# Kernel optimization log

Measured on AMD Instinct MI355X. Metric: run time of the kernel, lower is better.

Reference implementation:

```python
import jax, jax.numpy as jnp
import numpy as np

SQ, SK, D = 8192, 8192, 128

def setup_inputs() -> dict:
    k = jax.random.key(0)
    kq, kk, kv = jax.random.split(k, 3)
    query = jax.random.normal(kq, (SQ, D), dtype=jnp.float32)
    key = jax.random.normal(kk, (SK, D), dtype=jnp.float32)
    value = jax.random.normal(kv, (SK, D), dtype=jnp.float32)
    return {"query": query, "key": key, "value": value}

def reference(query, key, value):
    # attn_weights = dot_general(q, k, contract last dims) -> [Sq, Sk]
    attn_weights = jnp.einsum('qd,kd->qk', query, key)
    # softmax over key dims (second half of attn_weights dims)
    attn_weights = jax.nn.softmax(attn_weights, axis=-1)
    # dropout is identity: train=False -> deterministic
    # y = dot_general(attn_weights, value, contract key dims) -> [Sq, Dv]
    y = jnp.einsum('qk,kd->qd', attn_weights, value)
    return y
```

## Files before the change

kernel.cpp:

```cpp
#include <hip/hip_runtime.h>
#include <hip/hip_bf16.h>
#include <stdint.h>

#define SQ 8192
#define SK 8192
#define DH 128
#define NIT 32
#define L2E 1.4426950408889634f
#define CB 40.0f

typedef __attribute__((ext_vector_type(8))) _Float16 f16x8;
typedef __attribute__((ext_vector_type(8))) short bf16x8;
typedef __attribute__((ext_vector_type(16))) float f32x16;
typedef __attribute__((ext_vector_type(4))) short s16x4;
typedef __attribute__((ext_vector_type(4))) unsigned int u32x4;

__device__ __forceinline__ short f2h(float f) {
  _Float16 h = (_Float16)f;
  return __builtin_bit_cast(short, h);
}
__device__ __forceinline__ short f2bf(float f) {
  uint32_t u = __builtin_bit_cast(uint32_t, f);
  u = (u + 0x7FFFu + ((u >> 16) & 1u)) >> 16;
  return (short)u;
}

__global__ __launch_bounds__(256) void prep_kernel(const float* __restrict__ K,
                                                   const float* __restrict__ V,
                                                   short* __restrict__ Kimg,
                                                   short* __restrict__ Vimg) {
  __shared__ short T[32][136];
  const int tid = threadIdx.x;
  if (blockIdx.x < 256) {
    const int kb = blockIdx.x;
#pragma unroll
    for (int i = 0; i < 2; ++i) {
      int ci = i * 256 + tid;
      int kc = ci >> 6, lane = ci & 63;
      int key = kb * 32 + (lane & 31);
      int k0 = kc * 16 + (lane >> 5) * 8;
      const float* src = K + (size_t)key * DH + k0;
      float4 a = *(const float4*)src;
      float4 b = *(const float4*)(src + 4);
      s16x4 o0, o1;
      o0.x = f2h(a.x); o0.y = f2h(a.y); o0.z = f2h(a.z); o0.w = f2h(a.w);
      o1.x = f2h(b.x); o1.y = f2h(b.y); o1.z = f2h(b.z); o1.w = f2h(b.w);
      s16x4* dst = (s16x4*)(Kimg + (size_t)kb * 4096 + ci * 8);
      dst[0] = o0; dst[1] = o1;
    }
  } else {
    const int kb = blockIdx.x - 256;
#pragma unroll
    for (int i = 0; i < 4; ++i) {
      int fi = i * 256 + tid;
      int key = fi >> 5;
      int dc = (fi & 31) * 4;
      float4 v = ((const float4*)V)[(size_t)(kb * 32 + key) * (DH / 4) + (fi & 31)];
      T[key][dc + 0] = f2bf(v.x); T[key][dc + 1] = f2bf(v.y);
      T[key][dc + 2] = f2bf(v.z); T[key][dc + 3] = f2bf(v.w);
    }
    __syncthreads();
#pragma unroll
    for (int i = 0; i < 2; ++i) {
      int ci = i * 256 + tid;
      int lane = ci & 63;
      int g = ci >> 6;
      int dt = g & 3, ks = g >> 2;
      int base = ks * 16 + (lane >> 5) * 4;
      int d = dt * 32 + (lane & 31);
      s16x4 o0, o1;
      o0.x = T[base + 0][d]; o0.y = T[base + 1][d];
      o0.z = T[base + 2][d]; o0.w = T[base + 3][d];
      o1.x = T[base + 8][d]; o1.y = T[base + 9][d];
      o1.z = T[base + 10][d]; o1.w = T[base + 11][d];
      s16x4* dst = (s16x4*)(Vimg + (size_t)kb * 4096 + ci * 8);
      dst[0] = o0; dst[1] = o1;
    }
  }
}

__global__ __launch_bounds__(512, 2) void attn_kernel(const float* __restrict__ Q,
                                                      const short* __restrict__ Kimg,
                                                      const short* __restrict__ Vimg,
                                                      float* __restrict__ out) {
  __shared__ __align__(16) char smem[67584];
  const int tid = threadIdx.x;
  const int w = tid >> 6;
  const int lane = tid & 63;
  const int half = lane >> 5;
  const int l32 = lane & 31;
  const int qrow0 = blockIdx.x * 32;

  f16x8 qf[8];
  {
    const float* qp = Q + (size_t)(qrow0 + l32) * DH + half * 8;
#pragma unroll
    for (int kc = 0; kc < 8; ++kc) {
      float4 a = *(const float4*)(qp + kc * 16);
      float4 b = *(const float4*)(qp + kc * 16 + 4);
      f16x8 h;
      h[0] = (_Float16)a.x; h[1] = (_Float16)a.y; h[2] = (_Float16)a.z; h[3] = (_Float16)a.w;
      h[4] = (_Float16)b.x; h[5] = (_Float16)b.y; h[6] = (_Float16)b.z; h[7] = (_Float16)b.w;
      qf[kc] = h;
    }
  }

  f32x16 of[4];
#pragma unroll
  for (int dt = 0; dt < 4; ++dt)
#pragma unroll
    for (int c = 0; c < 16; ++c) of[dt][c] = 0.f;
  float l_lane = 0.f;

  f16x8 kf[8];
  bf16x8 vf[8];

  {
    const short* kp = Kimg + (size_t)w * 4096;
    const short* vp = Vimg + (size_t)w * 4096;
#pragma unroll
    for (int kc = 0; kc < 8; ++kc) kf[kc] = *(const f16x8*)(kp + kc * 512 + lane * 8);
#pragma unroll
    for (int g = 0; g < 8; ++g) vf[g] = *(const bf16x8*)(vp + g * 512 + lane * 8);
  }

  for (int t = 0; t < NIT; ++t) {
    f32x16 sacc;
#pragma unroll
    for (int c = 0; c < 16; ++c) sacc[c] = 0.f;
#pragma unroll
    for (int kc = 0; kc < 8; ++kc)
      sacc = __builtin_amdgcn_mfma_f32_32x32x16_f16(kf[kc], qf[kc], sacc, 0, 0, 0);

    if (t + 1 < NIT) {
      const short* kp = Kimg + (size_t)((t + 1) * 8 + w) * 4096;
#pragma unroll
      for (int kc = 0; kc < 8; ++kc) kf[kc] = *(const f16x8*)(kp + kc * 512 + lane * 8);
    }

    u32x4 pav0, pav1;
#pragma unroll
    for (int r = 0; r < 4; ++r) {
      float pA = __builtin_amdgcn_exp2f(fmaf(sacc[2 * r], L2E, -CB));
      float pB = __builtin_amdgcn_exp2f(fmaf(sacc[2 * r + 1], L2E, -CB));
      float pC = __builtin_amdgcn_exp2f(fmaf(sacc[8 + 2 * r], L2E, -CB));
      float pD = __builtin_amdgcn_exp2f(fmaf(sacc[8 + 2 * r + 1], L2E, -CB));
      l_lane += (pA + pB) + (pC + pD);
      uint32_t uA = __builtin_bit_cast(uint32_t, pA); uA += 0x7FFFu + ((uA >> 16) & 1u);
      uint32_t uB = __builtin_bit_cast(uint32_t, pB); uB += 0x7FFFu + ((uB >> 16) & 1u);
      uint32_t uC = __builtin_bit_cast(uint32_t, pC); uC += 0x7FFFu + ((uC >> 16) & 1u);
      uint32_t uD = __builtin_bit_cast(uint32_t, pD); uD += 0x7FFFu + ((uD >> 16) & 1u);
      pav0[r] = __builtin_amdgcn_perm(uB, uA, 0x07060302u);
      pav1[r] = __builtin_amdgcn_perm(uD, uC, 0x07060302u);
    }
    bf16x8 pa0 = __builtin_bit_cast(bf16x8, pav0);
    bf16x8 pa1 = __builtin_bit_cast(bf16x8, pav1);

#pragma unroll
    for (int dt = 0; dt < 4; ++dt) {
      of[dt] = __builtin_amdgcn_mfma_f32_32x32x16_bf16(pa0, vf[dt], of[dt], 0, 0, 0);
      of[dt] = __builtin_amdgcn_mfma_f32_32x32x16_bf16(pa1, vf[4 + dt], of[dt], 0, 0, 0);
    }

    if (t + 1 < NIT) {
      const short* vp = Vimg + (size_t)((t + 1) * 8 + w) * 4096;
#pragma unroll
      for (int g = 0; g < 8; ++g) vf[g] = *(const bf16x8*)(vp + g * 512 + lane * 8);
    }
  }

  float l_tot = l_lane + __shfl_xor(l_lane, 32);

  __syncthreads();
  float* mO = (float*)smem;
  float* R = mO + (w & 3) * 4224;
  if (w < 4) {
#pragma unroll
    for (int c = 0; c < 16; ++c) {
      const int row = (c & 3) + 8 * (c >> 2) + 4 * half;
      float* br = R + row * 132;
#pragma unroll
      for (int dt = 0; dt < 4; ++dt) br[dt * 32 + l32] = of[dt][c];
    }
    if (half == 0) R[l32 * 132 + 128] = l_tot;
  }
  __syncthreads();
  if (w >= 4) {
#pragma unroll
    for (int c = 0; c < 16; ++c) {
      const int row = (c & 3) + 8 * (c >> 2) + 4 * half;
      float* br = R + row * 132;
#pragma unroll
      for (int dt = 0; dt < 4; ++dt) br[dt * 32 + l32] += of[dt][c];
    }
    if (half == 0) R[l32 * 132 + 128] += l_tot;
  }
  __syncthreads();
  {
    const int row = tid >> 4;
    const int cg = tid & 15;
    float den = mO[row * 132 + 128] + mO[4224 + row * 132 + 128] +
                mO[8448 + row * 132 + 128] + mO[12672 + row * 132 + 128];
    float inv = 1.f / den;
    float4 s0 = {0.f, 0.f, 0.f, 0.f}, s1 = {0.f, 0.f, 0.f, 0.f};
#pragma unroll
    for (int rg = 0; rg < 4; ++rg) {
      const float* p = mO + rg * 4224 + row * 132 + cg * 8;
      float4 a = *(const float4*)p;
      float4 b = *(const float4*)(p + 4);
      s0.x += a.x; s0.y += a.y; s0.z += a.z; s0.w += a.w;
      s1.x += b.x; s1.y += b.y; s1.z += b.z; s1.w += b.w;
    }
    s0.x *= inv; s0.y *= inv; s0.z *= inv; s0.w *= inv;
    s1.x *= inv; s1.y *= inv; s1.z *= inv; s1.w *= inv;
    float* op = out + (size_t)(qrow0 + row) * DH + cg * 8;
    *(float4*)op = s0;
    *(float4*)(op + 4) = s1;
  }
}

extern "C" void kernel_launch(void* const* d_in, const int* in_sizes, int n_in,
                              void* d_out, int out_size, void* d_ws, size_t ws_size,
                              hipStream_t stream) {
  const float* Q = (const float*)d_in[0];
  const float* K = (const float*)d_in[1];
  const float* V = (const float*)d_in[2];
  float* out = (float*)d_out;
  short* Kimg = (short*)d_ws;
  short* Vimg = (short*)d_ws + (size_t)SK * DH;
  prep_kernel<<<512, 256, 0, stream>>>(K, V, Kimg, Vimg);
  attn_kernel<<<SQ / 32, 512, 0, stream>>>(Q, Kimg, Vimg, out);
}
```

Before: 110.8 us.

## Split keys across blocks, share K tiles via LDS, add combine kernel

Each block now handles 64 query rows over half the key range. Two query groups of waves share K tiles that are staged into LDS with double-buffered global_load_lds, which halves K global traffic per query row. Partial outputs and row sums are written to the workspace, and a separate combine kernel merges them and normalises. The change also splits the QK MFMA chain into two independent accumulators and raises wave priority around the MFMA sections. In exchange it adds a per-iteration __syncthreads, V loads that are no longer prefetched, an extra kernel launch, and extra global traffic for the partial results.

```diff
diff --git a/kernel.cpp b/kernel.cpp
--- a/kernel.cpp
+++ b/kernel.cpp
@@ -23,6 +23,12 @@
   uint32_t u = __builtin_bit_cast(uint32_t, f);
   u = (u + 0x7FFFu + ((u >> 16) & 1u)) >> 16;
   return (short)u;
+}
+
+__device__ __forceinline__ void gl_lds16(const void* g, void* l) {
+  __builtin_amdgcn_global_load_lds(
+      (const __attribute__((address_space(1))) void*)g,
+      (__attribute__((address_space(3))) void*)l, 16, 0, 0);
 }
 
 __global__ __launch_bounds__(256) void prep_kernel(const float* __restrict__ K,
@@ -79,17 +85,26 @@
   }
 }
 
-__global__ __launch_bounds__(512, 2) void attn_kernel(const float* __restrict__ Q,
-                                                      const short* __restrict__ Kimg,
-                                                      const short* __restrict__ Vimg,
-                                                      float* __restrict__ out) {
+__global__ __launch_bounds__(512, 2) void attn_split(const float* __restrict__ Q,
+                                                     const short* __restrict__ Kimg,
+                                                     const short* __restrict__ Vimg,
+                                                     float* __restrict__ Oa,
+                                                     float* __restrict__ Ob,
+                                                     float* __restrict__ l0,
+                                                     float* __restrict__ l1) {
   __shared__ __align__(16) char smem[67584];
+  short* stg = (short*)smem;
   const int tid = threadIdx.x;
   const int w = tid >> 6;
   const int lane = tid & 63;
   const int half = lane >> 5;
   const int l32 = lane & 31;
-  const int qrow0 = blockIdx.x * 32;
+  const int qh = w >> 2;
+  const int ks = w & 3;
+  const int qb = blockIdx.x >> 1;
+  const int kh = blockIdx.x & 1;
+  const int qrow0 = qb * 64 + qh * 32;
+  const int kb0 = kh * 128;
 
   f16x8 qf[8];
   {
@@ -112,31 +127,49 @@
     for (int c = 0; c < 16; ++c) of[dt][c] = 0.f;
   float l_lane = 0.f;
 
-  f16x8 kf[8];
-  bf16x8 vf[8];
-
-  {
-    const short* kp = Kimg + (size_t)w * 4096;
-    const short* vp = Vimg + (size_t)w * 4096;
-#pragma unroll
-    for (int kc = 0; kc < 8; ++kc) kf[kc] = *(const f16x8*)(kp + kc * 512 + lane * 8);
-#pragma unroll
-    for (int g = 0; g < 8; ++g) vf[g] = *(const bf16x8*)(vp + g * 512 + lane * 8);
-  }
+  const short* gK = Kimg + ((size_t)kb0 + (w >> 1)) * 4096 + (w & 1) * 2048 + lane * 8;
+  short* lK = stg + (w >> 1) * 4096 + (w & 1) * 2048;
+
+  auto STAGE = [&](int c, int t) {
+    const short* g = gK + (size_t)t * 16384;
+    short* l = lK + c * 16384;
+#pragma unroll
+    for (int j = 0; j < 4; ++j)
+      gl_lds16(g + j * 512, l + j * 512);
+  };
+
+  STAGE(0, 0);
+  __syncthreads();
+  int cur = 0;
 
   for (int t = 0; t < NIT; ++t) {
+    bf16x8 vf[8];
+    {
+      const short* vp = Vimg + ((size_t)kb0 + t * 4 + ks) * 4096 + lane * 8;
+#pragma unroll
+      for (int g2 = 0; g2 < 8; ++g2) vf[g2] = *(const bf16x8*)(vp + g2 * 512);
+    }
+
+    const short* bk = stg + cur * 16384 + ks * 4096 + lane * 8;
+    f16x8 kf[8];
+#pragma unroll
+    for (int kc = 0; kc < 8; ++kc) kf[kc] = *(const f16x8*)(bk + kc * 512);
+
+    if (t + 1 < NIT) STAGE(cur ^ 1, t + 1);
+
+    f32x16 sa, sb;
+#pragma unroll
+    for (int c = 0; c < 16; ++c) { sa[c] = 0.f; sb[c] = 0.f; }
+    __builtin_amdgcn_s_setprio(1);
+#pragma unroll
+    for (int kc = 0; kc < 4; ++kc) {
+      sa = __builtin_amdgcn_mfma_f32_32x32x16_f16(kf[kc], qf[kc], sa, 0, 0, 0);
+      sb = __builtin_amdgcn_mfma_f32_32x32x16_f16(kf[4 + kc], qf[4 + kc], sb, 0, 0, 0);
+    }
+    __builtin_amdgcn_s_setprio(0);
     f32x16 sacc;
 #pragma unroll
-    for (int c = 0; c < 16; ++c) sacc[c] = 0.f;
-#pragma unroll
-    for (int kc = 0; kc < 8; ++kc)
-      sacc = __builtin_amdgcn_mfma_f32_32x32x16_f16(kf[kc], qf[kc], sacc, 0, 0, 0);
-
-    if (t + 1 < NIT) {
-      const short* kp = Kimg + (size_t)((t + 1) * 8 + w) * 4096;
-#pragma unroll
-      for (int kc = 0; kc < 8; ++kc) kf[kc] = *(const f16x8*)(kp + kc * 512 + lane * 8);
-    }
+    for (int c = 0; c < 16; ++c) sacc[c] = sa[c] + sb[c];
 
     u32x4 pav0, pav1;
 #pragma unroll
@@ -156,25 +189,24 @@
     bf16x8 pa0 = __builtin_bit_cast(bf16x8, pav0);
     bf16x8 pa1 = __builtin_bit_cast(bf16x8, pav1);
 
+    __builtin_amdgcn_s_setprio(1);
 #pragma unroll
     for (int dt = 0; dt < 4; ++dt) {
       of[dt] = __builtin_amdgcn_mfma_f32_32x32x16_bf16(pa0, vf[dt], of[dt], 0, 0, 0);
       of[dt] = __builtin_amdgcn_mfma_f32_32x32x16_bf16(pa1, vf[4 + dt], of[dt], 0, 0, 0);
     }
-
-    if (t + 1 < NIT) {
-      const short* vp = Vimg + (size_t)((t + 1) * 8 + w) * 4096;
-#pragma unroll
-      for (int g = 0; g < 8; ++g) vf[g] = *(const bf16x8*)(vp + g * 512 + lane * 8);
-    }
+    __builtin_amdgcn_s_setprio(0);
+
+    __syncthreads();
+    cur ^= 1;
   }
 
   float l_tot = l_lane + __shfl_xor(l_lane, 32);
 
   __syncthreads();
   float* mO = (float*)smem;
-  float* R = mO + (w & 3) * 4224;
-  if (w < 4) {
+  float* R = mO + (qh * 2 + (ks & 1)) * 4224;
+  if (ks < 2) {
 #pragma unroll
     for (int c = 0; c < 16; ++c) {
       const int row = (c & 3) + 8 * (c >> 2) + 4 * half;
@@ -185,7 +217,7 @@
     if (half == 0) R[l32 * 132 + 128] = l_tot;
   }
   __syncthreads();
-  if (w >= 4) {
+  if (ks >= 2) {
 #pragma unroll
     for (int c = 0; c < 16; ++c) {
       const int row = (c & 3) + 8 * (c >> 2) + 4 * half;
@@ -197,26 +229,40 @@
   }
   __syncthreads();
   {
-    const int row = tid >> 4;
-    const int cg = tid & 15;
-    float den = mO[row * 132 + 128] + mO[4224 + row * 132 + 128] +
-                mO[8448 + row * 132 + 128] + mO[12672 + row * 132 + 128];
-    float inv = 1.f / den;
-    float4 s0 = {0.f, 0.f, 0.f, 0.f}, s1 = {0.f, 0.f, 0.f, 0.f};
-#pragma unroll
-    for (int rg = 0; rg < 4; ++rg) {
-      const float* p = mO + rg * 4224 + row * 132 + cg * 8;
-      float4 a = *(const float4*)p;
-      float4 b = *(const float4*)(p + 4);
-      s0.x += a.x; s0.y += a.y; s0.z += a.z; s0.w += a.w;
-      s1.x += b.x; s1.y += b.y; s1.z += b.z; s1.w += b.w;
-    }
-    s0.x *= inv; s0.y *= inv; s0.z *= inv; s0.w *= inv;
-    s1.x *= inv; s1.y *= inv; s1.z *= inv; s1.w *= inv;
-    float* op = out + (size_t)(qrow0 + row) * DH + cg * 8;
-    *(float4*)op = s0;
-    *(float4*)(op + 4) = s1;
-  }
+    const int row = tid >> 3;
+    const int cg = tid & 7;
+    const int qh2 = row >> 5;
+    const int r32 = row & 31;
+    const float* Ra = mO + (qh2 * 2 + 0) * 4224 + r32 * 132;
+    const float* Rb = mO + (qh2 * 2 + 1) * 4224 + r32 * 132;
+    float lp = Ra[128] + Rb[128];
+    float* dst = (kh ? Ob : Oa) + (size_t)(qb * 64 + row) * DH + cg * 16;
+#pragma unroll
+    for (int k = 0; k < 4; ++k) {
+      float4 a = *(const float4*)(Ra + cg * 16 + k * 4);
+      float4 b = *(const float4*)(Rb + cg * 16 + k * 4);
+      a.x += b.x; a.y += b.y; a.z += b.z; a.w += b.w;
+      *(float4*)(dst + k * 4) = a;
+    }
+    if (cg == 0) (kh ? l1 : l0)[qb * 64 + row] = lp;
+  }
+}
+
+__global__ __launch_bounds__(256) void combine_kernel(float* __restrict__ Oa,
+                                                      const float* __restrict__ Ob,
+                                                      const float* __restrict__ l0,
+                                                      const float* __restrict__ l1) {
+  const int idx = blockIdx.x * 256 + threadIdx.x;
+  const int row = idx >> 5;
+  const int c4 = (idx & 31) * 4;
+  const float inv = 1.f / (l0[row] + l1[row]);
+  float* pa = Oa + (size_t)row * DH + c4;
+  const float* pb = Ob + (size_t)row * DH + c4;
+  float4 a = *(const float4*)pa;
+  float4 b = *(const float4*)pb;
+  a.x = (a.x + b.x) * inv; a.y = (a.y + b.y) * inv;
+  a.z = (a.z + b.z) * inv; a.w = (a.w + b.w) * inv;
+  *(float4*)pa = a;
 }
 
 extern "C" void kernel_launch(void* const* d_in, const int* in_sizes, int n_in,
@@ -226,8 +272,13 @@
   const float* K = (const float*)d_in[1];
   const float* V = (const float*)d_in[2];
   float* out = (float*)d_out;
-  short* Kimg = (short*)d_ws;
-  short* Vimg = (short*)d_ws + (size_t)SK * DH;
+  char* ws = (char*)d_ws;
+  short* Kimg = (short*)ws;
+  short* Vimg = (short*)(ws + 2097152);
+  float* Ob = (float*)(ws + 4194304);
+  float* l0 = (float*)(ws + 8388608);
+  float* l1 = l0 + SQ;
   prep_kernel<<<512, 256, 0, stream>>>(K, V, Kimg, Vimg);
-  attn_kernel<<<SQ / 32, 512, 0, stream>>>(Q, Kimg, Vimg, out);
-}
+  attn_split<<<SQ / 64 * 2, 512, 0, stream>>>(Q, Kimg, Vimg, out, Ob, l0, l1);
+  combine_kernel<<<SQ * DH / 4 / 256, 256, 0, stream>>>(out, Ob, l0, l1);
+}
```

Result: slower. 118.9 us (+7.4%).

## Split key range across two blocks per query tile and combine partials

Applied to the files above, without the earlier changes.

The attention kernel now splits the key sequence into two halves. Each half is handled by its own workgroup, which doubles the grid to 512 blocks so the 256 compute units are better occupied. Each block writes unnormalized partial outputs and row sums, and a new combine kernel adds the two halves and normalizes. This works without rescaling because the softmax uses a fixed offset rather than a running max. The cost is an extra launch, plus global traffic for the partial outputs and sums, and launch bounds are raised to 4 waves-per-EU hint.

```diff
diff --git a/kernel.cpp b/kernel.cpp
--- a/kernel.cpp
+++ b/kernel.cpp
@@ -5,7 +5,7 @@
 #define SQ 8192
 #define SK 8192
 #define DH 128
-#define NIT 32
+#define NIT 16
 #define L2E 1.4426950408889634f
 #define CB 40.0f
 
@@ -79,17 +79,24 @@
   }
 }
 
-__global__ __launch_bounds__(512, 2) void attn_kernel(const float* __restrict__ Q,
-                                                      const short* __restrict__ Kimg,
-                                                      const short* __restrict__ Vimg,
-                                                      float* __restrict__ out) {
+__global__ __launch_bounds__(512, 4) void attn_split(const float* __restrict__ Q,
+                                                     const short* __restrict__ Kimg,
+                                                     const short* __restrict__ Vimg,
+                                                     float* __restrict__ Oa,
+                                                     float* __restrict__ Ob,
+                                                     float* __restrict__ l0,
+                                                     float* __restrict__ l1) {
   __shared__ __align__(16) char smem[67584];
   const int tid = threadIdx.x;
   const int w = tid >> 6;
   const int lane = tid & 63;
   const int half = lane >> 5;
   const int l32 = lane & 31;
-  const int qrow0 = blockIdx.x * 32;
+  const int b = blockIdx.x;
+  const int kh = (b >> 2) & 1;
+  const int qb = (b >> 3) * 4 + (b & 3);
+  const int qrow0 = qb * 32;
+  const int kb0 = kh * 128;
 
   f16x8 qf[8];
   {
@@ -97,10 +104,10 @@
 #pragma unroll
     for (int kc = 0; kc < 8; ++kc) {
       float4 a = *(const float4*)(qp + kc * 16);
-      float4 b = *(const float4*)(qp + kc * 16 + 4);
+      float4 b2 = *(const float4*)(qp + kc * 16 + 4);
       f16x8 h;
       h[0] = (_Float16)a.x; h[1] = (_Float16)a.y; h[2] = (_Float16)a.z; h[3] = (_Float16)a.w;
-      h[4] = (_Float16)b.x; h[5] = (_Float16)b.y; h[6] = (_Float16)b.z; h[7] = (_Float16)b.w;
+      h[4] = (_Float16)b2.x; h[5] = (_Float16)b2.y; h[6] = (_Float16)b2.z; h[7] = (_Float16)b2.w;
       qf[kc] = h;
     }
   }
@@ -116,8 +123,8 @@
   bf16x8 vf[8];
 
   {
-    const short* kp = Kimg + (size_t)w * 4096;
-    const short* vp = Vimg + (size_t)w * 4096;
+    const short* kp = Kimg + (size_t)(kb0 + w) * 4096;
+    const short* vp = Vimg + (size_t)(kb0 + w) * 4096;
 #pragma unroll
     for (int kc = 0; kc < 8; ++kc) kf[kc] = *(const f16x8*)(kp + kc * 512 + lane * 8);
 #pragma unroll
@@ -133,7 +140,7 @@
       sacc = __builtin_amdgcn_mfma_f32_32x32x16_f16(kf[kc], qf[kc], sacc, 0, 0, 0);
 
     if (t + 1 < NIT) {
-      const short* kp = Kimg + (size_t)((t + 1) * 8 + w) * 4096;
+      const short* kp = Kimg + (size_t)(kb0 + (t + 1) * 8 + w) * 4096;
 #pragma unroll
       for (int kc = 0; kc < 8; ++kc) kf[kc] = *(const f16x8*)(kp + kc * 512 + lane * 8);
     }
@@ -163,7 +170,7 @@
     }
 
     if (t + 1 < NIT) {
-      const short* vp = Vimg + (size_t)((t + 1) * 8 + w) * 4096;
+      const short* vp = Vimg + (size_t)(kb0 + (t + 1) * 8 + w) * 4096;
 #pragma unroll
       for (int g = 0; g < 8; ++g) vf[g] = *(const bf16x8*)(vp + g * 512 + lane * 8);
     }
@@ -199,24 +206,39 @@
   {
     const int row = tid >> 4;
     const int cg = tid & 15;
-    float den = mO[row * 132 + 128] + mO[4224 + row * 132 + 128] +
-                mO[8448 + row * 132 + 128] + mO[12672 + row * 132 + 128];
-    float inv = 1.f / den;
+    float lp = mO[row * 132 + 128] + mO[4224 + row * 132 + 128] +
+               mO[8448 + row * 132 + 128] + mO[12672 + row * 132 + 128];
     float4 s0 = {0.f, 0.f, 0.f, 0.f}, s1 = {0.f, 0.f, 0.f, 0.f};
 #pragma unroll
     for (int rg = 0; rg < 4; ++rg) {
       const float* p = mO + rg * 4224 + row * 132 + cg * 8;
       float4 a = *(const float4*)p;
-      float4 b = *(const float4*)(p + 4);
+      float4 b2 = *(const float4*)(p + 4);
       s0.x += a.x; s0.y += a.y; s0.z += a.z; s0.w += a.w;
-      s1.x += b.x; s1.y += b.y; s1.z += b.z; s1.w += b.w;
-    }
-    s0.x *= inv; s0.y *= inv; s0.z *= inv; s0.w *= inv;
-    s1.x *= inv; s1.y *= inv; s1.z *= inv; s1.w *= inv;
-    float* op = out + (size_t)(qrow0 + row) * DH + cg * 8;
+      s1.x += b2.x; s1.y += b2.y; s1.z += b2.z; s1.w += b2.w;
+    }
+    float* op = (kh ? Ob : Oa) + (size_t)(qrow0 + row) * DH + cg * 8;
     *(float4*)op = s0;
     *(float4*)(op + 4) = s1;
-  }
+    if (cg == 0) (kh ? l1 : l0)[qrow0 + row] = lp;
+  }
+}
+
+__global__ __launch_bounds__(256) void combine_kernel(float* __restrict__ Oa,
+                                                      const float* __restrict__ Ob,
+                                                      const float* __restrict__ l0,
+                                                      const float* __restrict__ l1) {
+  const int idx = blockIdx.x * 256 + threadIdx.x;
+  const int row = idx >> 5;
+  const int c4 = (idx & 31) * 4;
+  const float inv = 1.f / (l0[row] + l1[row]);
+  float* pa = Oa + (size_t)row * DH + c4;
+  const float* pb = Ob + (size_t)row * DH + c4;
+  float4 a = *(const float4*)pa;
+  float4 b = *(const float4*)pb;
+  a.x = (a.x + b.x) * inv; a.y = (a.y + b.y) * inv;
+  a.z = (a.z + b.z) * inv; a.w = (a.w + b.w) * inv;
+  *(float4*)pa = a;
 }
 
 extern "C" void kernel_launch(void* const* d_in, const int* in_sizes, int n_in,
@@ -226,8 +248,13 @@
   const float* K = (const float*)d_in[1];
   const float* V = (const float*)d_in[2];
   float* out = (float*)d_out;
-  short* Kimg = (short*)d_ws;
-  short* Vimg = (short*)d_ws + (size_t)SK * DH;
+  char* ws = (char*)d_ws;
+  short* Kimg = (short*)ws;
+  short* Vimg = (short*)(ws + 2097152);
+  float* Ob = (float*)(ws + 4194304);
+  float* l0 = (float*)(ws + 8388608);
+  float* l1 = l0 + SQ;
   prep_kernel<<<512, 256, 0, stream>>>(K, V, Kimg, Vimg);
-  attn_kernel<<<SQ / 32, 512, 0, stream>>>(Q, Kimg, Vimg, out);
-}
+  attn_split<<<512, 512, 0, stream>>>(Q, Kimg, Vimg, out, Ob, l0, l1);
+  combine_kernel<<<SQ * DH / 4 / 256, 256, 0, stream>>>(out, Ob, l0, l1);
+}
```

Result: slower. 321.8 us (+190.5%).
